# Kernel optimization log

Measured on AMD Instinct MI355X. Metric: run time of the kernel, lower is better.

Reference implementation:

```python
import jax, jax.numpy as jnp
import numpy as np


def _segsum(x):
    """x: (..., T) -> (..., T, T) with [i,j] = sum_{k=j+1..i} x[k] for i>=j else -inf."""
    T = x.shape[-1]
    i = jnp.arange(T)
    strict_lower = i[:, None] > i[None, :]
    xx = jnp.where(strict_lower, x[..., :, None], 0.0)
    s = jnp.cumsum(xx, axis=-2)
    return jnp.where(i[:, None] >= i[None, :], s, -jnp.inf)


def setup_inputs() -> dict:
    key = jax.random.key(0)
    kX, kA, kB, kC = jax.random.split(key, 4)
    b, S, h, p, n = 8, 4096, 16, 64, 64
    X = jax.random.normal(kX, (b, S, h, p), jnp.float32)
    # decay-like A (negative) keeps exp(cumsum) finite at seq 4096; same math as module
    A = -jnp.abs(jax.random.normal(kA, (b, S, h), jnp.float32)) * 0.1
    B = jax.random.normal(kB, (b, S, h, n), jnp.float32)
    C = jax.random.normal(kC, (b, S, h, n), jnp.float32)
    initial_states = jnp.zeros((b, 1, h, p, n), jnp.float32)
    return {"X": X, "initial_states": initial_states, "A": A, "B": B, "C": C, "chunk_size": 64}


def reference(X, initial_states, A, B, C, chunk_size):
    b, S, h, p = X.shape
    n = B.shape[-1]
    c = S // chunk_size
    l = chunk_size
    # chunk: b (c l) ... -> b c l ...
    Xc = X.reshape(b, c, l, h, p)
    Bc = B.reshape(b, c, l, h, n)
    Cc = C.reshape(b, c, l, h, n)
    Ac = A.reshape(b, c, l, h).transpose(0, 3, 1, 2)  # b h c l
    A_cumsum = jnp.cumsum(Ac, axis=-1)                 # b h c l
    # 1. intra-chunk (diagonal) output
    Lm = jnp.exp(_segsum(Ac))                          # b h c l l
    Y_diag = jnp.einsum('bclhn,bcshn,bhcls,bcshp->bclhp', Cc, Bc, Lm, Xc)
    # 2. per-chunk states
    decay_states = jnp.exp(A_cumsum[..., -1:] - A_cumsum)  # b h c l
    states = jnp.einsum('bclhn,bhcl,bclhp->bchpn', Bc, decay_states, Xc)
    # 3. inter-chunk recurrence (via chunk-level segsum)
    states = jnp.concatenate([initial_states, states], axis=1)  # b (c+1) h p n
    A_last = jnp.pad(A_cumsum[..., -1], ((0, 0), (0, 0), (1, 0)))  # b h (c+1)
    decay_chunk = jnp.exp(_segsum(A_last))                         # b h (c+1) (c+1)
    new_states = jnp.einsum('bhzc,bchpn->bzhpn', decay_chunk, states)
    states = new_states[:, :-1]  # b c h p n (final_state = new_states[:, -1], unused)
    # 4. state -> output
    state_decay_out = jnp.exp(A_cumsum)  # b h c l
    Y_off = jnp.einsum('bclhn,bchpn,bhcl->bclhp', Cc, states, state_decay_out)
    return (Y_diag + Y_off).reshape(b, S, h, p)
```

## Files before the change

kernel.cpp:

```cpp
#include <hip/hip_runtime.h>


typedef __bf16 bf16x4 __attribute__((ext_vector_type(4)));
typedef __bf16 bf16x8 __attribute__((ext_vector_type(8)));
typedef float  f32x4  __attribute__((ext_vector_type(4)));

constexpr int LDT = 72;

__device__ __forceinline__ f32x4 mfma16(bf16x8 a, bf16x8 b, f32x4 c) {
    return __builtin_amdgcn_mfma_f32_16x16x32_bf16(a, b, c, 0, 0, 0);
}
__device__ __forceinline__ void bar_lds() {
    asm volatile("s_waitcnt lgkmcnt(0)\n\ts_barrier" ::: "memory");
}
__device__ __forceinline__ int swz(int row, int byteoff) {
    return byteoff ^ (((row >> 2) & 7) << 4);
}

struct SMemF {
    __bf16 Cm[2][64][LDT];
    __bf16 Bm[2][64][LDT];
    __bf16 Bt[2][64][LDT];
    __bf16 Mm[2][64][LDT];
    __bf16 Xt[3][32][LDT];
    __bf16 St16[2][32][LDT];
    float  St32[32][68];
    float  sY[2][64][36];
    float  ds[4][64];
    float  dout[4][64];
    float  douti[4][64];
    float  dlast[4];
};

__global__ void ssd_fused(const float* __restrict__ Xg, const float* __restrict__ Ig,
                          const float* __restrict__ Ag, const float* __restrict__ Bg,
                          const float* __restrict__ Cg, float* __restrict__ Yg)
{
    const int ph = blockIdx.x, hh = blockIdx.y, bb = blockIdx.z;
    const int tid = threadIdx.x;
    const int wid = tid >> 6, lane = tid & 63;
    const int fr = lane & 15, fg = lane >> 4;
    const int iw2 = (wid >> 1) * 16;
    const int pt  = (wid & 1) * 16;
    const int jh  = (wid & 1) * 32;

    __shared__ __align__(16) SMemF sm;
    const size_t tbase = (size_t)bb * 4096;

    const int half = tid >> 8;
    const int u    = tid & 255;
    const int lt0  = (u >> 4) * 4;
    const int rr0  = u >> 4;
    const int cq0  = (u & 15) * 4;
    const int xl  = tid >> 3;
    const int xp4 = (tid & 7) * 4;
    const int sp  = tid >> 4;
    const int sn4 = (tid & 15) * 4;

    float rb[4][4], rx[4];
    float aA = 0.0f;

    auto scan_to = [&](float v, int tb) {
        #pragma unroll
        for (int o = 1; o < 64; o <<= 1) { float t = __shfl_up(v, o, 64); if (lane >= o) v += t; }
        const float last = __shfl(v, 63, 64);
        sm.ds[tb][lane]    = expf(last - v);
        sm.dout[tb][lane]  = expf(v);
        sm.douti[tb][lane] = expf(v - last);
        if (lane == 63) sm.dlast[tb] = expf(v);
    };

    {
        const size_t iofs = (((size_t)bb*16 + hh)*64 + (ph*32 + sp))*(size_t)64 + sn4;
        const float4 v = *reinterpret_cast<const float4*>(&Ig[iofs]);
        sm.St32[sp][sn4+0] = v.x; sm.St32[sp][sn4+1] = v.y;
        sm.St32[sp][sn4+2] = v.z; sm.St32[sp][sn4+3] = v.w;
        *reinterpret_cast<bf16x4*>(&sm.St16[0][sp][sn4]) =
            (bf16x4){(__bf16)v.x, (__bf16)v.y, (__bf16)v.z, (__bf16)v.w};
    }
    #pragma unroll
    for (int j = 0; j < 4; ++j) {
        const int row = (half == 0) ? (lt0 + j) : (rr0 + 16*j);
        const size_t go = ((tbase + row)*16 + hh)*(size_t)64 + cq0;
        *reinterpret_cast<float4*>(rb[j]) = (half == 0)
            ? *reinterpret_cast<const float4*>(&Bg[go])
            : *reinterpret_cast<const float4*>(&Cg[go]);
    }
    *reinterpret_cast<float4*>(rx) =
        *reinterpret_cast<const float4*>(&Xg[((tbase + xl)*16 + hh)*(size_t)64 + ph*32 + xp4]);
    if (wid < 2) {
        const float v = Ag[(tbase + wid*64 + lane)*16 + hh];
        scan_to(v, wid);
    }
    if (half == 0) {
        #pragma unroll
        for (int j = 0; j < 4; ++j)
            *reinterpret_cast<bf16x4*>(&sm.Bm[0][lt0 + j][cq0]) =
                (bf16x4){(__bf16)rb[j][0], (__bf16)rb[j][1], (__bf16)rb[j][2], (__bf16)rb[j][3]};
        #pragma unroll
        for (int q = 0; q < 4; ++q)
            *reinterpret_cast<bf16x4*>(
                reinterpret_cast<char*>(&sm.Bt[0][cq0 + q][0]) + swz(cq0 + q, lt0*2)) =
                (bf16x4){(__bf16)rb[0][q], (__bf16)rb[1][q], (__bf16)rb[2][q], (__bf16)rb[3][q]};
    } else {
        #pragma unroll
        for (int j = 0; j < 4; ++j)
            *reinterpret_cast<bf16x4*>(&sm.Cm[0][rr0 + 16*j][cq0]) =
                (bf16x4){(__bf16)rb[j][0], (__bf16)rb[j][1], (__bf16)rb[j][2], (__bf16)rb[j][3]};
    }
    bar_lds();
    {
        const float dsl = sm.ds[0][xl];
        #pragma unroll
        for (int q = 0; q < 4; ++q)
            *reinterpret_cast<__bf16*>(
                reinterpret_cast<char*>(&sm.Xt[0][xp4 + q][0]) + swz(xp4 + q, xl*2)) =
                (__bf16)(rx[q] * dsl);
    }
    #pragma unroll
    for (int j = 0; j < 4; ++j) {
        const int row = (half == 0) ? (lt0 + j) : (rr0 + 16*j);
        const size_t go = ((tbase + 64 + row)*16 + hh)*(size_t)64 + cq0;
        *reinterpret_cast<float4*>(rb[j]) = (half == 0)
            ? *reinterpret_cast<const float4*>(&Bg[go])
            : *reinterpret_cast<const float4*>(&Cg[go]);
    }
    *reinterpret_cast<float4*>(rx) =
        *reinterpret_cast<const float4*>(&Xg[((tbase + 64 + xl)*16 + hh)*(size_t)64 + ph*32 + xp4]);
    if (wid == 0) aA = Ag[(tbase + 2*64 + lane)*16 + hh];
    bar_lds();

    f32x4 aoprev = {};
    int x0 = 0, x1 = 1, x2 = 2;

    for (int c = 0; c < 64; ++c) {
        const int ci = c & 1, nb = ci ^ 1;
        const int t0 = c & 3, t1 = (c+1) & 3, t2 = (c+2) & 3, t3 = (c+3) & 3;

        f32x4 g0 = {}, g1 = {}, aoacc = {}, stacc = {};
        #pragma unroll
        for (int ks = 0; ks < 2; ++ks) {
            const int k0 = ks*32 + fg*8;
            const bf16x8 aC  = *reinterpret_cast<const bf16x8*>(&sm.Cm[ci][iw2 + fr][k0]);
            const bf16x8 bB0 = *reinterpret_cast<const bf16x8*>(&sm.Bm[ci][jh      + fr][k0]);
            const bf16x8 bB1 = *reinterpret_cast<const bf16x8*>(&sm.Bm[ci][jh + 16 + fr][k0]);
            const bf16x8 bSt = *reinterpret_cast<const bf16x8*>(&sm.St16[ci][pt + fr][k0]);
            const bf16x8 aBt = *reinterpret_cast<const bf16x8*>(
                reinterpret_cast<const char*>(&sm.Bt[ci][iw2 + fr][0]) + swz(iw2 + fr, k0*2));
            const bf16x8 bXt = *reinterpret_cast<const bf16x8*>(
                reinterpret_cast<const char*>(&sm.Xt[x0][pt + fr][0]) + swz(pt + fr, k0*2));
            g0    = mfma16(aC,  bB0, g0);
            g1    = mfma16(aC,  bB1, g1);
            aoacc = mfma16(aC,  bSt, aoacc);
            stacc = mfma16(aBt, bXt, stacc);
        }
        f32x4 ad = {};
        if (c > 0) {
            #pragma unroll
            for (int ks = 0; ks < 2; ++ks) {
                const int k0 = ks*32 + fg*8;
                const bf16x8 aM = *reinterpret_cast<const bf16x8*>(&sm.Mm[nb][iw2 + fr][k0]);
                const bf16x8 bX = *reinterpret_cast<const bf16x8*>(
                    reinterpret_cast<const char*>(&sm.Xt[x2][pt + fr][0]) + swz(pt + fr, k0*2));
                ad = mfma16(aM, bX, ad);
            }
        }
        if (c <= 61 && wid == 0) scan_to(aA, t2);
        if (c >= 2) {
            const float4 v = *reinterpret_cast<const float4*>(&sm.sY[nb][xl][xp4]);
            *reinterpret_cast<float4*>(
                &Yg[((tbase + (size_t)(c-2)*64 + xl)*16 + hh)*(size_t)64 + ph*32 + xp4]) = v;
        }
        if (c < 63) {
            if (half == 0) {
                #pragma unroll
                for (int j = 0; j < 4; ++j)
                    *reinterpret_cast<bf16x4*>(&sm.Bm[nb][lt0 + j][cq0]) =
                        (bf16x4){(__bf16)rb[j][0], (__bf16)rb[j][1], (__bf16)rb[j][2], (__bf16)rb[j][3]};
                #pragma unroll
                for (int q = 0; q < 4; ++q)
                    *reinterpret_cast<bf16x4*>(
                        reinterpret_cast<char*>(&sm.Bt[nb][cq0 + q][0]) + swz(cq0 + q, lt0*2)) =
                        (bf16x4){(__bf16)rb[0][q], (__bf16)rb[1][q], (__bf16)rb[2][q], (__bf16)rb[3][q]};
            } else {
                #pragma unroll
                for (int j = 0; j < 4; ++j)
                    *reinterpret_cast<bf16x4*>(&sm.Cm[nb][rr0 + 16*j][cq0]) =
                        (bf16x4){(__bf16)rb[j][0], (__bf16)rb[j][1], (__bf16)rb[j][2], (__bf16)rb[j][3]};
            }
            const float dsl = sm.ds[t1][xl];
            #pragma unroll
            for (int q = 0; q < 4; ++q)
                *reinterpret_cast<__bf16*>(
                    reinterpret_cast<char*>(&sm.Xt[x1][xp4 + q][0]) + swz(xp4 + q, xl*2)) =
                    (__bf16)(rx[q] * dsl);
        }
        if (c < 62) {
            const size_t s2 = tbase + (size_t)(c + 2)*64;
            #pragma unroll
            for (int j = 0; j < 4; ++j) {
                const int row = (half == 0) ? (lt0 + j) : (rr0 + 16*j);
                const size_t go = ((s2 + row)*16 + hh)*(size_t)64 + cq0;
                *reinterpret_cast<float4*>(rb[j]) = (half == 0)
                    ? *reinterpret_cast<const float4*>(&Bg[go])
                    : *reinterpret_cast<const float4*>(&Cg[go]);
            }
            *reinterpret_cast<float4*>(rx) =
                *reinterpret_cast<const float4*>(&Xg[((s2 + xl)*16 + hh)*(size_t)64 + ph*32 + xp4]);
        }
        if (wid == 0 && c <= 60) aA = Ag[(tbase + (size_t)(c + 3)*64 + lane)*16 + hh];
        if (c > 0) {
            #pragma unroll
            for (int r = 0; r < 4; ++r) {
                const int i = iw2 + fg*4 + r;
                sm.sY[ci][i][pt + fr] = ad[r] + sm.dout[t3][i] * aoprev[r];
            }
        }
        #pragma unroll
        for (int jt = 0; jt < 2; ++jt) {
            const int j = jh + jt*16 + fr;
            const f32x4& gg = jt ? g1 : g0;
            #pragma unroll
            for (int r = 0; r < 4; ++r) {
                const int i = iw2 + fg*4 + r;
                const float val = (i >= j) ? gg[r] * sm.douti[t0][i] : 0.0f;
                sm.Mm[ci][i][j] = (__bf16)val;
            }
        }
        if (c < 63) {
            const float dl = sm.dlast[t0];
            const int p = pt + fr, n0 = iw2 + fg*4;
            const float4 ov = *reinterpret_cast<const float4*>(&sm.St32[p][n0]);
            float4 nv;
            nv.x = fmaf(dl, ov.x, stacc[0]); nv.y = fmaf(dl, ov.y, stacc[1]);
            nv.z = fmaf(dl, ov.z, stacc[2]); nv.w = fmaf(dl, ov.w, stacc[3]);
            *reinterpret_cast<float4*>(&sm.St32[p][n0]) = nv;
            *reinterpret_cast<bf16x4*>(&sm.St16[nb][p][n0]) =
                (bf16x4){(__bf16)nv.x, (__bf16)nv.y, (__bf16)nv.z, (__bf16)nv.w};
        }
        aoprev = aoacc;
        bar_lds();
        const int xt = x0; x0 = x1; x1 = x2; x2 = xt;
    }

    {
        f32x4 ad = {};
        #pragma unroll
        for (int ks = 0; ks < 2; ++ks) {
            const int k0 = ks*32 + fg*8;
            const bf16x8 aM = *reinterpret_cast<const bf16x8*>(&sm.Mm[1][iw2 + fr][k0]);
            const bf16x8 bX = *reinterpret_cast<const bf16x8*>(
                reinterpret_cast<const char*>(&sm.Xt[x2][pt + fr][0]) + swz(pt + fr, k0*2));
            ad = mfma16(aM, bX, ad);
        }
        #pragma unroll
        for (int r = 0; r < 4; ++r) {
            const int i = iw2 + fg*4 + r;
            sm.sY[0][i][pt + fr] = ad[r] + sm.dout[3][i] * aoprev[r];
        }
    }
    {
        const float4 v = *reinterpret_cast<const float4*>(&sm.sY[1][xl][xp4]);
        *reinterpret_cast<float4*>(
            &Yg[((tbase + (size_t)62*64 + xl)*16 + hh)*(size_t)64 + ph*32 + xp4]) = v;
    }
    bar_lds();
    {
        const float4 v = *reinterpret_cast<const float4*>(&sm.sY[0][xl][xp4]);
        *reinterpret_cast<float4*>(
            &Yg[((tbase + (size_t)63*64 + xl)*16 + hh)*(size_t)64 + ph*32 + xp4]) = v;
    }
}

extern "C" void kernel_launch(void* const* d_in, const int* in_sizes, int n_in,
                              void* d_out, int out_size, void* d_ws, size_t ws_size,
                              hipStream_t stream) {
    const float* X  = (const float*)d_in[0];
    const float* I  = (const float*)d_in[1];
    const float* A  = (const float*)d_in[2];
    const float* Bp = (const float*)d_in[3];
    const float* Cp = (const float*)d_in[4];
    float* Y = (float*)d_out;
    ssd_fused<<<dim3(2, 16, 8), 512, 0, stream>>>(X, I, A, Bp, Cp, Y);
}
```

Measured before the change: 132.8 us.

## Double-buffer global prefetch registers and issue loads at chunk start

Splits the staging registers into two sets (A/B) and unrolls the chunk loop by two so the global loads for chunk c+2 are issued at the very start of each phase, before the MFMA work, instead of after the LDS stores. A sched_barrier keeps the compiler from sinking the loads. This gives the memory latency a full phase of compute to hide behind, at the cost of doubling the prefetch register footprint, which may raise VGPR pressure and reduce occupancy.

```diff
diff --git a/kernel.cpp b/kernel.cpp
--- a/kernel.cpp
+++ b/kernel.cpp
@@ -57,8 +57,10 @@
     const int sp  = tid >> 4;
     const int sn4 = (tid & 15) * 4;
 
-    float rb[4][4], rx[4];
+    float rbA[4][4], rxA[4], rbB[4][4], rxB[4];
     float aA = 0.0f;
+    f32x4 aoprev = {};
+    int x0 = 0, x1 = 1, x2 = 2;
 
     auto scan_to = [&](float v, int tb) {
         #pragma unroll
@@ -82,11 +84,11 @@
     for (int j = 0; j < 4; ++j) {
         const int row = (half == 0) ? (lt0 + j) : (rr0 + 16*j);
         const size_t go = ((tbase + row)*16 + hh)*(size_t)64 + cq0;
-        *reinterpret_cast<float4*>(rb[j]) = (half == 0)
+        *reinterpret_cast<float4*>(rbA[j]) = (half == 0)
             ? *reinterpret_cast<const float4*>(&Bg[go])
             : *reinterpret_cast<const float4*>(&Cg[go]);
     }
-    *reinterpret_cast<float4*>(rx) =
+    *reinterpret_cast<float4*>(rxA) =
         *reinterpret_cast<const float4*>(&Xg[((tbase + xl)*16 + hh)*(size_t)64 + ph*32 + xp4]);
     if (wid < 2) {
         const float v = Ag[(tbase + wid*64 + lane)*16 + hh];
@@ -96,17 +98,17 @@
         #pragma unroll
         for (int j = 0; j < 4; ++j)
             *reinterpret_cast<bf16x4*>(&sm.Bm[0][lt0 + j][cq0]) =
-                (bf16x4){(__bf16)rb[j][0], (__bf16)rb[j][1], (__bf16)rb[j][2], (__bf16)rb[j][3]};
+                (bf16x4){(__bf16)rbA[j][0], (__bf16)rbA[j][1], (__bf16)rbA[j][2], (__bf16)rbA[j][3]};
         #pragma unroll
         for (int q = 0; q < 4; ++q)
             *reinterpret_cast<bf16x4*>(
                 reinterpret_cast<char*>(&sm.Bt[0][cq0 + q][0]) + swz(cq0 + q, lt0*2)) =
-                (bf16x4){(__bf16)rb[0][q], (__bf16)rb[1][q], (__bf16)rb[2][q], (__bf16)rb[3][q]};
+                (bf16x4){(__bf16)rbA[0][q], (__bf16)rbA[1][q], (__bf16)rbA[2][q], (__bf16)rbA[3][q]};
     } else {
         #pragma unroll
         for (int j = 0; j < 4; ++j)
             *reinterpret_cast<bf16x4*>(&sm.Cm[0][rr0 + 16*j][cq0]) =
-                (bf16x4){(__bf16)rb[j][0], (__bf16)rb[j][1], (__bf16)rb[j][2], (__bf16)rb[j][3]};
+                (bf16x4){(__bf16)rbA[j][0], (__bf16)rbA[j][1], (__bf16)rbA[j][2], (__bf16)rbA[j][3]};
     }
     bar_lds();
     {
@@ -115,27 +117,40 @@
         for (int q = 0; q < 4; ++q)
             *reinterpret_cast<__bf16*>(
                 reinterpret_cast<char*>(&sm.Xt[0][xp4 + q][0]) + swz(xp4 + q, xl*2)) =
-                (__bf16)(rx[q] * dsl);
+                (__bf16)(rxA[q] * dsl);
     }
     #pragma unroll
     for (int j = 0; j < 4; ++j) {
         const int row = (half == 0) ? (lt0 + j) : (rr0 + 16*j);
         const size_t go = ((tbase + 64 + row)*16 + hh)*(size_t)64 + cq0;
-        *reinterpret_cast<float4*>(rb[j]) = (half == 0)
+        *reinterpret_cast<float4*>(rbB[j]) = (half == 0)
             ? *reinterpret_cast<const float4*>(&Bg[go])
             : *reinterpret_cast<const float4*>(&Cg[go]);
     }
-    *reinterpret_cast<float4*>(rx) =
+    *reinterpret_cast<float4*>(rxB) =
         *reinterpret_cast<const float4*>(&Xg[((tbase + 64 + xl)*16 + hh)*(size_t)64 + ph*32 + xp4]);
     if (wid == 0) aA = Ag[(tbase + 2*64 + lane)*16 + hh];
     bar_lds();
 
-    f32x4 aoprev = {};
-    int x0 = 0, x1 = 1, x2 = 2;
-
-    for (int c = 0; c < 64; ++c) {
-        const int ci = c & 1, nb = ci ^ 1;
+    auto phase = [&](int c, int ci, float (&rbW)[4][4], float (&rxW)[4],
+                     float (&rbR)[4][4], float (&rxR)[4]) {
+        const int nb = ci ^ 1;
         const int t0 = c & 3, t1 = (c+1) & 3, t2 = (c+2) & 3, t3 = (c+3) & 3;
+
+        if (c < 62) {
+            const size_t s2 = tbase + (size_t)(c + 2)*64;
+            #pragma unroll
+            for (int j = 0; j < 4; ++j) {
+                const int row = (half == 0) ? (lt0 + j) : (rr0 + 16*j);
+                const size_t go = ((s2 + row)*16 + hh)*(size_t)64 + cq0;
+                *reinterpret_cast<float4*>(rbW[j]) = (half == 0)
+                    ? *reinterpret_cast<const float4*>(&Bg[go])
+                    : *reinterpret_cast<const float4*>(&Cg[go]);
+            }
+            *reinterpret_cast<float4*>(rxW) =
+                *reinterpret_cast<const float4*>(&Xg[((s2 + xl)*16 + hh)*(size_t)64 + ph*32 + xp4]);
+        }
+        __builtin_amdgcn_sched_barrier(0);
 
         f32x4 g0 = {}, g1 = {}, aoacc = {}, stacc = {};
         #pragma unroll
@@ -176,37 +191,27 @@
                 #pragma unroll
                 for (int j = 0; j < 4; ++j)
                     *reinterpret_cast<bf16x4*>(&sm.Bm[nb][lt0 + j][cq0]) =
-                        (bf16x4){(__bf16)rb[j][0], (__bf16)rb[j][1], (__bf16)rb[j][2], (__bf16)rb[j][3]};
+                        (bf16x4){(__bf16)rbR[j][0], (__bf16)rbR[j][1],
+                                 (__bf16)rbR[j][2], (__bf16)rbR[j][3]};
                 #pragma unroll
                 for (int q = 0; q < 4; ++q)
                     *reinterpret_cast<bf16x4*>(
                         reinterpret_cast<char*>(&sm.Bt[nb][cq0 + q][0]) + swz(cq0 + q, lt0*2)) =
-                        (bf16x4){(__bf16)rb[0][q], (__bf16)rb[1][q], (__bf16)rb[2][q], (__bf16)rb[3][q]};
+                        (bf16x4){(__bf16)rbR[0][q], (__bf16)rbR[1][q],
+                                 (__bf16)rbR[2][q], (__bf16)rbR[3][q]};
             } else {
                 #pragma unroll
                 for (int j = 0; j < 4; ++j)
                     *reinterpret_cast<bf16x4*>(&sm.Cm[nb][rr0 + 16*j][cq0]) =
-                        (bf16x4){(__bf16)rb[j][0], (__bf16)rb[j][1], (__bf16)rb[j][2], (__bf16)rb[j][3]};
+                        (bf16x4){(__bf16)rbR[j][0], (__bf16)rbR[j][1],
+                                 (__bf16)rbR[j][2], (__bf16)rbR[j][3]};
             }
             const float dsl = sm.ds[t1][xl];
             #pragma unroll
             for (int q = 0; q < 4; ++q)
                 *reinterpret_cast<__bf16*>(
                     reinterpret_cast<char*>(&sm.Xt[x1][xp4 + q][0]) + swz(xp4 + q, xl*2)) =
-                    (__bf16)(rx[q] * dsl);
-        }
-        if (c < 62) {
-            const size_t s2 = tbase + (size_t)(c + 2)*64;
-            #pragma unroll
-            for (int j = 0; j < 4; ++j) {
-                const int row = (half == 0) ? (lt0 + j) : (rr0 + 16*j);
-                const size_t go = ((s2 + row)*16 + hh)*(size_t)64 + cq0;
-                *reinterpret_cast<float4*>(rb[j]) = (half == 0)
-                    ? *reinterpret_cast<const float4*>(&Bg[go])
-                    : *reinterpret_cast<const float4*>(&Cg[go]);
-            }
-            *reinterpret_cast<float4*>(rx) =
-                *reinterpret_cast<const float4*>(&Xg[((s2 + xl)*16 + hh)*(size_t)64 + ph*32 + xp4]);
+                    (__bf16)(rxR[q] * dsl);
         }
         if (wid == 0 && c <= 60) aA = Ag[(tbase + (size_t)(c + 3)*64 + lane)*16 + hh];
         if (c > 0) {
@@ -241,6 +246,11 @@
         aoprev = aoacc;
         bar_lds();
         const int xt = x0; x0 = x1; x1 = x2; x2 = xt;
+    };
+
+    for (int cb = 0; cb < 64; cb += 2) {
+        phase(cb,     0, rbA, rxA, rbB, rxB);
+        phase(cb + 1, 1, rbB, rxB, rbA, rxA);
     }
 
     {
```

New measurement: 290.6 us. 2.19x slower.
